# Kernel optimization log

Measured on AMD Instinct MI355X. Metric: run time of the kernel, lower is better.

The kernel has to match this reference:

```python
import jax, jax.numpy as jnp
import numpy as np

ALPHA = 0.1
MAX_ITER = 35
TOL = 0.01
STEP = ALPHA / 2.0  # step_size = alpha/2 as in TV2DFunction.forward


def _prox_tv1d(step, y):
    """Exact 1D TV prox via taut-string lower/upper hulls (faithful port of _prox_tv1d)."""
    n = y.shape[0]
    width = n + 1
    dt = y.dtype
    cs = jnp.cumsum(y)
    y_low = jnp.concatenate([jnp.zeros(1, dt), cs - step]).at[width - 1].add(step)
    y_up = jnp.concatenate([jnp.zeros(1, dt), cs + step]).at[width - 1].add(-step)

    inf = jnp.asarray(jnp.inf, dt)
    il = jnp.zeros(width, jnp.int32)   # index_low
    iu = jnp.zeros(width, jnp.int32)   # index_up
    idx = jnp.zeros(width, jnp.int32)  # breakpoint indices
    sl = jnp.zeros(width, dt).at[0].set(inf)    # slope_low
    su = jnp.zeros(width, dt).at[0].set(-inf)   # slope_up
    z = jnp.zeros(width, dt)
    zero = jnp.int32(0)

    def fdiv(num, a, b):
        # a > b always holds on the taken branch; maximum() only guards the
        # unselected jnp.where branch against NaN/Inf.
        return num / jnp.maximum(a - b, 1).astype(dt)

    def body(i, st):
        il, sl, iu, su, idx, z, s_l, c_l, s_u, c_u, c = st
        c_l = c_l + 1
        c_u = c_u + 1
        il = il.at[c_l].set(i)
        iu = iu.at[c_u].set(i)
        sl = sl.at[c_l].set(y_low[i] - y_low[i - 1])

        def w1_cond(t):
            il_, sl_, c_l_ = t
            return (c_l_ > s_l + 1) & (sl_[jnp.maximum(s_l, c_l_ - 1)] <= sl_[c_l_])

        def w1_body(t):
            il_, sl_, c_l_ = t
            c_l_ = c_l_ - 1
            il_ = il_.at[c_l_].set(i)
            ns = jnp.where(c_l_ > s_l + 1,
                           fdiv(y_low[i] - y_low[il_[c_l_ - 1]], i, il_[c_l_ - 1]),
                           fdiv(y_low[i] - z[c], i, idx[c]))
            return il_, sl_.at[c_l_].set(ns), c_l_

        il, sl, c_l = jax.lax.while_loop(w1_cond, w1_body, (il, sl, c_l))

        su = su.at[c_u].set(y_up[i] - y_up[i - 1])

        def w2_cond(t):
            iu_, su_, c_u_ = t
            return (c_u_ > s_u + 1) & (su_[jnp.maximum(s_u, c_u_ - 1)] >= su_[c_u_])

        def w2_body(t):
            iu_, su_, c_u_ = t
            c_u_ = c_u_ - 1
            iu_ = iu_.at[c_u_].set(i)
            ns = jnp.where(c_u_ > s_u + 1,
                           fdiv(y_up[i] - y_up[iu_[c_u_ - 1]], i, iu_[c_u_ - 1]),
                           fdiv(y_up[i] - z[c], i, idx[c]))
            return iu_, su_.at[c_u_].set(ns), c_u_

        iu, su, c_u = jax.lax.while_loop(w2_cond, w2_body, (iu, su, c_u))

        def w3_cond(t):
            idx_, z_, sl_, il_, s_u_, c_ = t
            return (c_l == s_l + 1) & (c_u > s_u_ + 1) & (sl_[c_l] >= su[s_u_ + 1])

        def w3_body(t):
            idx_, z_, sl_, il_, s_u_, c_ = t
            c_ = c_ + 1
            s_u_ = s_u_ + 1
            k = iu[s_u_]
            idx_ = idx_.at[c_].set(k)
            z_ = z_.at[c_].set(y_up[k])
            il_ = il_.at[s_l].set(k)
            sl_ = sl_.at[c_l].set(fdiv(y_low[i] - y_up[k], i, k))
            return idx_, z_, sl_, il_, s_u_, c_

        idx, z, sl, il, s_u, c = jax.lax.while_loop(w3_cond, w3_body, (idx, z, sl, il, s_u, c))

        def w4_cond(t):
            idx_, z_, su_, iu_, s_l_, c_ = t
            return (c_u == s_u + 1) & (c_l > s_l_ + 1) & (su_[c_u] <= sl[s_l_ + 1])

        def w4_body(t):
            idx_, z_, su_, iu_, s_l_, c_ = t
            c_ = c_ + 1
            s_l_ = s_l_ + 1
            k = il[s_l_]
            idx_ = idx_.at[c_].set(k)
            z_ = z_.at[c_].set(y_low[k])
            iu_ = iu_.at[s_u].set(k)
            su_ = su_.at[c_u].set(fdiv(y_up[i] - y_low[k], i, k))
            return idx_, z_, su_, iu_, s_l_, c_

        idx, z, su, iu, s_l, c = jax.lax.while_loop(w4_cond, w4_body, (idx, z, su, iu, s_l, c))

        return il, sl, iu, su, idx, z, s_l, c_l, s_u, c_u, c

    st = (il, sl, iu, su, idx, z, zero, zero, zero, zero, zero)
    il, sl, iu, su, idx, z, s_l, c_l, s_u, c_u, c = jax.lax.fori_loop(1, width, body, st)

    # tail: append remaining lower-hull points to the breakpoint list
    m = c_l - s_l
    offs = jnp.arange(width)
    valid = (offs >= 1) & (offs <= m)
    src = il[jnp.clip(s_l + offs, 0, width - 1)]
    tgt = jnp.where(valid, c + offs, width)  # 'width' is out of bounds -> dropped
    idx = idx.at[tgt].set(src, mode='drop')
    z = z.at[tgt].set(y_low[src], mode='drop')
    c = c + m

    # piecewise-constant output: slope of taut string on each segment
    a = (z - jnp.roll(z, 1)) / jnp.maximum(idx - jnp.roll(idx, 1), 1).astype(dt)
    knots = jnp.where(offs <= c, idx, n + 1)  # sorted; idx[c] == n
    seg = jnp.searchsorted(knots, jnp.arange(n), side='right')  # segment id in [1, c]
    return a[seg]


def _prox_cols(step, A):
    return jax.vmap(lambda col: _prox_tv1d(step, col), in_axes=1, out_axes=1)(A)


def _prox_rows(step, A):
    return jax.vmap(lambda row: _prox_tv1d(step, row))(A)


def _prox_tv2d(x, step, max_iter, tol):
    """Douglas-Rachford splitting for 2D TV prox (Barbero & Sra 2014)."""
    def cond(carry):
        it, x_, p, q, acc = carry
        return (it < max_iter) & (acc >= tol)

    def body(carry):
        it, x_, p, q, _ = carry
        y = _prox_cols(step, x_ + p)
        p = p + x_ - y
        x2 = _prox_rows(step, y + q)
        q = q + y - x2
        acc = jnp.max(jnp.abs(y - x2))
        return it + 1, x2, p, q, acc

    z0 = jnp.zeros_like(x)
    init = (jnp.int32(0), x, z0, z0, jnp.asarray(jnp.inf, x.dtype))
    return jax.lax.while_loop(cond, body, init)[1]


def setup_inputs() -> dict:
    key = jax.random.key(0)
    X = jax.random.normal(key, (256, 256), dtype=jnp.float32)
    return {"X": X}


def reference(X):
    return _prox_tv2d(X, STEP, MAX_ITER, TOL)
```

## Files before the change

kernel.cpp:

```cpp
#include <hip/hip_runtime.h>

#define N 256
#define NB 256
#define NT 64
#define LAM 0.05f
#define TWOLAM (2.0f * LAM)
#define FOURLAM (4.0f * LAM)
#define MAXIT 35
#define TOL 0.01f
#define SLOTSTRIDE 2
#define POLLBUDGET (1 << 17)

typedef unsigned long long u64;

__device__ __forceinline__ float rlane(float v, int lane) {
    return __int_as_float(__builtin_amdgcn_readlane(__float_as_int(v), lane));
}

__device__ __forceinline__ void gstore(float* p, float v) {
    __hip_atomic_store(p, v, __ATOMIC_RELAXED, __HIP_MEMORY_SCOPE_AGENT);
}
__device__ __forceinline__ u64 ald(const u64* p) {
    return __hip_atomic_load(p, __ATOMIC_RELAXED, __HIP_MEMORY_SCOPE_AGENT);
}
__device__ __forceinline__ void ast(u64* p, u64 v) {
    __hip_atomic_store(p, v, __ATOMIC_RELAXED, __HIP_MEMORY_SCOPE_AGENT);
}

__device__ __forceinline__ void gload_col(const float* mat, int c, int lane, float& a,
                                          float& b, float& d, float& e) {
    const float* p0 = mat + (size_t)lane * N + c;
    const float* p1 = p0 + 64 * N;
    const float* p2 = p0 + 128 * N;
    const float* p3 = p0 + 192 * N;
    asm volatile("global_load_dword %0, %4, off sc0 sc1\n\t"
                 "global_load_dword %1, %5, off sc0 sc1\n\t"
                 "global_load_dword %2, %6, off sc0 sc1\n\t"
                 "global_load_dword %3, %7, off sc0 sc1\n\t"
                 "s_waitcnt vmcnt(0)"
                 : "=&v"(a), "=&v"(b), "=&v"(d), "=&v"(e)
                 : "v"(p0), "v"(p1), "v"(p2), "v"(p3)
                 : "memory");
}

struct Dist { float r0, r1, r2, r3; };

__device__ __forceinline__ float dfetch(const Dist& d, int k) {
    const int lane = k & 63;
    const int sel = k >> 6;
    float a = rlane(d.r0, lane);
    float b = rlane(d.r1, lane);
    float c = rlane(d.r2, lane);
    float e = rlane(d.r3, lane);
    float ab = (sel & 1) ? b : a;
    float ce = (sel & 1) ? e : c;
    return (sel & 2) ? ce : ab;
}

__device__ __forceinline__ void flushseg(Dist& o, int lo, int hi, float val, int lane) {
    const unsigned len = (unsigned)(hi - lo);
    const int base = lane - lo;
    o.r0 = ((unsigned)(base      ) <= len) ? val : o.r0;
    o.r1 = ((unsigned)(base + 64 ) <= len) ? val : o.r1;
    o.r2 = ((unsigned)(base + 128) <= len) ? val : o.r2;
    o.r3 = ((unsigned)(base + 192) <= len) ? val : o.r3;
}

__device__ __forceinline__ u64 sel4(u64 a, u64 b, u64 c, u64 d, int r) {
    u64 ab = (r & 1) ? b : a;
    u64 cd = (r & 1) ? d : c;
    return (r & 2) ? cd : ab;
}

__device__ __forceinline__ unsigned wredmax(unsigned x) {
    unsigned t;
    t = (unsigned)__builtin_amdgcn_update_dpp(0, (int)x, 0x111, 0xf, 0xf, true); x = x > t ? x : t;
    t = (unsigned)__builtin_amdgcn_update_dpp(0, (int)x, 0x112, 0xf, 0xf, true); x = x > t ? x : t;
    t = (unsigned)__builtin_amdgcn_update_dpp(0, (int)x, 0x114, 0xf, 0xf, true); x = x > t ? x : t;
    t = (unsigned)__builtin_amdgcn_update_dpp(0, (int)x, 0x118, 0xf, 0xf, true); x = x > t ? x : t;
    t = (unsigned)__builtin_amdgcn_update_dpp(0, (int)x, 0x142, 0xf, 0xf, true); x = x > t ? x : t;
    t = (unsigned)__builtin_amdgcn_update_dpp(0, (int)x, 0x143, 0xf, 0xf, true); x = x > t ? x : t;
    return (unsigned)__builtin_amdgcn_readlane((int)x, 63);
}

__device__ __forceinline__ void pollcol(const u64* m, int c, unsigned seq, int lane, Dist& v) {
    const u64* p0 = m + (size_t)lane * N + c;
    const u64* p1 = p0 + 64 * N;
    const u64* p2 = p0 + 128 * N;
    const u64* p3 = p0 + 192 * N;
    u64 f0 = ald(p0), f1 = ald(p1), f2 = ald(p2), f3 = ald(p3);
    int spin = 0;
    for (;;) {
        u64 g0 = ald(p0), g1 = ald(p1), g2 = ald(p2), g3 = ald(p3);
        const bool ok = ((unsigned)f0 >= seq) & ((unsigned)f1 >= seq) &
                        ((unsigned)f2 >= seq) & ((unsigned)f3 >= seq);
        if (__all((int)ok)) break;
        if (__builtin_expect(++spin > POLLBUDGET, 0)) break;
        f0 = g0; f1 = g1; f2 = g2; f3 = g3;
    }
    v.r0 = __uint_as_float((unsigned)(f0 >> 32));
    v.r1 = __uint_as_float((unsigned)(f1 >> 32));
    v.r2 = __uint_as_float((unsigned)(f2 >> 32));
    v.r3 = __uint_as_float((unsigned)(f3 >> 32));
}

__device__ __forceinline__ void storerow(u64* m, int row, unsigned seq, const Dist& o, int lane) {
    u64* r = m + (size_t)row * N;
    ast(r + lane,       ((u64)__float_as_uint(o.r0) << 32) | (u64)seq);
    ast(r + lane + 64,  ((u64)__float_as_uint(o.r1) << 32) | (u64)seq);
    ast(r + lane + 128, ((u64)__float_as_uint(o.r2) << 32) | (u64)seq);
    ast(r + lane + 192, ((u64)__float_as_uint(o.r3) << 32) | (u64)seq);
}

__device__ void tv1d_scan(const Dist& v, Dist& o, const int lane)
{
    const float lam = LAM, mlam = -LAM, twolam = TWOLAM;

    Dist vnx;
    {
        float a0 = __shfl_down(v.r0, 1), a1 = __shfl_down(v.r1, 1);
        float a2 = __shfl_down(v.r2, 1), a3 = __shfl_down(v.r3, 1);
        const bool hi = (lane == 63);
        vnx.r0 = hi ? rlane(v.r1, 0) : a0;
        vnx.r1 = hi ? rlane(v.r2, 0) : a1;
        vnx.r2 = hi ? rlane(v.r3, 0) : a2;
        vnx.r3 = hi ? v.r3 : a3;
    }
    Dist d;
    d.r0 = vnx.r0 - v.r0;  d.r1 = vnx.r1 - v.r1;
    d.r2 = vnx.r2 - v.r2;  d.r3 = vnx.r3 - v.r3;
    const unsigned lambits = __float_as_uint(lam);
    Dist sl;
    sl.r0 = __uint_as_float((__float_as_uint(d.r0) & 0x80000000u) | lambits);
    sl.r1 = __uint_as_float((__float_as_uint(d.r1) & 0x80000000u) | lambits);
    sl.r2 = __uint_as_float((__float_as_uint(d.r2) & 0x80000000u) | lambits);
    sl.r3 = __uint_as_float((__float_as_uint(d.r3) & 0x80000000u) | lambits);
    Dist slp;
    {
        float b0 = __shfl_up(sl.r0, 1), b1 = __shfl_up(sl.r1, 1);
        float b2 = __shfl_up(sl.r2, 1), b3 = __shfl_up(sl.r3, 1);
        const bool lo = (lane == 0);
        slp.r0 = lo ? 0.0f : b0;
        slp.r1 = lo ? rlane(sl.r0, 63) : b1;
        slp.r2 = lo ? rlane(sl.r1, 63) : b2;
        slp.r3 = lo ? rlane(sl.r2, 63) : b3;
    }
    Dist e, g;
    {
        float t0 = v.r0 - slp.r0, t1 = v.r1 - slp.r1, t2 = v.r2 - slp.r2, t3 = v.r3 - slp.r3;
        e.r0 = t0 + sl.r0;  e.r1 = t1 + sl.r1;  e.r2 = t2 + sl.r2;  e.r3 = t3 + sl.r3;
        g.r0 = t0 - lam;    g.r1 = t1 - lam;    g.r2 = t2 - lam;    g.r3 = t3 - lam;
    }
    const u64 S0 = __ballot(d.r0 < 0.0f);
    const u64 S1 = __ballot(d.r1 < 0.0f);
    const u64 S2 = __ballot(d.r2 < 0.0f);
    const u64 S3 = __ballot(d.r3 < 0.0f);
    const u64 B20 = __ballot(fabsf(d.r0) > TWOLAM);
    const u64 B21 = __ballot(fabsf(d.r1) > TWOLAM);
    const u64 B22 = __ballot(fabsf(d.r2) > TWOLAM);
    const u64 B23 = __ballot(fabsf(d.r3) > TWOLAM);
    const u64 B40 = __ballot(fabsf(d.r0) > FOURLAM);
    const u64 B41 = __ballot(fabsf(d.r1) > FOURLAM);
    const u64 B42 = __ballot(fabsf(d.r2) > FOURLAM);
    const u64 B43 = __ballot(fabsf(d.r3) > FOURLAM);
    const u64 Sp0 = (S0 << 1);
    const u64 Sp1 = (S1 << 1) | (S0 >> 63);
    const u64 Sp2 = (S2 << 1) | (S1 >> 63);
    const u64 Sp3 = (S3 << 1) | (S2 >> 63);
    const u64 NF0 = ~(B40 | (B20 & ~(S0 ^ Sp0)));
    const u64 NF1 = ~(B41 | (B21 & ~(S1 ^ Sp1)));
    const u64 NF2 = ~(B42 | (B22 & ~(S2 ^ Sp2)));
    const u64 NF3 = ~((B43 | (B23 & ~(S3 ^ Sp3))) & 0x7FFFFFFFFFFFFFFFull);
    const u64 FNn0 = (S0 & B20) | (~S0 & B40);
    const u64 FNn1 = (S1 & B21) | (~S1 & B41);
    const u64 FNn2 = (S2 & B22) | (~S2 & B42);
    const u64 FNn3 = (S3 & B23) | (~S3 & B43);
    const u64 FNp0 = (~S0 & B20) | (S0 & B40);
    const u64 FNp1 = (~S1 & B21) | (S1 & B41);
    const u64 FNp2 = (~S2 & B22) | (S2 & B42);
    const u64 FNp3 = (~S3 & B23) | (S3 & B43);
    const int initFF = (int)(B40 & 1ull);

    auto firstnf = [&](int jmin) -> int {
        const int w = jmin >> 6;
        u64 m = sel4(NF0, NF1, NF2, NF3, w) >> (jmin & 63);
        if (m) return jmin + (int)__builtin_ctzll(m);
        u64 m1 = (w < 1) ? NF1 : 0ull;
        u64 m2 = (w < 2) ? NF2 : 0ull;
        if (m1) return 64 + (int)__builtin_ctzll(m1);
        if (m2) return 128 + (int)__builtin_ctzll(m2);
        return 192 + (int)__builtin_ctzll(NF3);
    };

    auto trigbit = [&](int kk, int neg) -> int {
        const int w = kk >> 6;
        const u64 m = neg ? sel4(FNn0, FNn1, FNn2, FNn3, w)
                          : sel4(FNp0, FNp1, FNp2, FNp3, w);
        return (int)((m >> (kk & 63)) & 1ull);
    };

    int k = 0, k0 = 0, km = 0, kp = 0;
    float umin = lam, umax = mlam;
    const float v0 = rlane(v.r0, 0);
    float vmin = v0 - lam, vmax = v0 + lam;
    float flen = 1.0f;
    float rnext = 0.5f;
    float vn1 = rlane(vnx.r0, 0);

    auto fastfwd = [&]() {
        const int K1 = firstnf(k + 1);
        const int sneg = (int)((sel4(S0, S1, S2, S3, k >> 6) >> (k & 63)) & 1ull);
        flushseg(o, k, k, sneg ? vmin : vmax, lane);
        if (K1 > k + 1) {
            const int lo = k + 1;
            const unsigned len = (unsigned)(K1 - 1 - lo);
            const int base = lane - lo;
            o.r0 = ((unsigned)(base      ) <= len) ? e.r0 : o.r0;
            o.r1 = ((unsigned)(base + 64 ) <= len) ? e.r1 : o.r1;
            o.r2 = ((unsigned)(base + 128) <= len) ? e.r2 : o.r2;
            o.r3 = ((unsigned)(base + 192) <= len) ? e.r3 : o.r3;
        }
        k = K1; k0 = K1; km = K1; kp = K1;
        vmin = dfetch(g, K1);
        vmax = vmin + twolam;
        umin = lam; umax = mlam;
        flen = 1.0f; rnext = 0.5f;
        vn1 = dfetch(vnx, K1);
    };

    auto do_step = [&]() {
        const float un = umin + vn1 - vmin;
        const float ux = umax + vn1 - vmax;
        const bool neg = un < mlam;
        const bool pos = ux > lam;
        const int wn = (k + 1) >> 6, bn = (k + 1) & 63;
        const int tn = (int)((sel4(FNn0, FNn1, FNn2, FNn3, wn) >> bn) & 1ull);
        const int tp = (int)((sel4(FNp0, FNp1, FNp2, FNp3, wn) >> bn) & 1ull);
        if (__builtin_expect((int)(neg | pos), 1)) {
            const float fval = neg ? vmin : vmax;
            const int   fhi  = neg ? km : kp;
            flushseg(o, k0, fhi, fval, lane);
            const int k0n = fhi + 1;
            float vstar;
            int trig;
            if (__builtin_expect((int)(k0n <= k), 0)) {
                vstar = dfetch(v, k0n);
                trig = trigbit(k0n, (int)neg);
            } else {
                vstar = vn1;
                trig = neg ? tn : tp;
            }
            k = k0n; k0 = k0n; km = k0n; kp = k0n;
            vmin = neg ? vstar : vstar - twolam;
            vmax = vmin + twolam;
            umin = lam; umax = mlam;
            flen = 1.0f; rnext = 0.5f;
            if (k < N - 1 && trig) {
                fastfwd();
            } else {
                vn1 = dfetch(vnx, k);
            }
        } else {
            k++;
            const float r = rnext;
            flen += 1.0f;
            const bool cmin = (un >= lam);
            const bool cmax = (ux <= mlam);
            vmin = cmin ? fmaf(un - lam, r, vmin) : vmin;
            km   = cmin ? k : km;
            umin = cmin ? lam : un;
            vmax = cmax ? fmaf(ux + lam, r, vmax) : vmax;
            kp   = cmax ? k : kp;
            umax = cmax ? mlam : ux;
            vn1 = dfetch(vnx, k);
            rnext = __builtin_amdgcn_rcpf(flen + 1.0f);
        }
    };

    if (initFF) fastfwd();

    for (;;) {
        while (k < N - 1) {
            do_step();
            if (k >= N - 1) break;
            do_step();
        }
        for (;;) {
            if (umin < 0.0f) {
                flushseg(o, k0, km, vmin, lane);
                k0 = km + 1;
                if (k0 > N - 1) return;
                km = k = k0;
                vmin = dfetch(v, k0);
                umin = lam;
                umax = vmin + lam - vmax;
                flen = 1.0f;
            } else if (umax > 0.0f) {
                flushseg(o, k0, kp, vmax, lane);
                k0 = kp + 1;
                if (k0 > N - 1) return;
                kp = k = k0;
                vmax = dfetch(v, k0);
                umax = mlam;
                umin = vmax - lam - vmin;
                flen = 1.0f;
            } else {
                vmin += umin / flen;
                flushseg(o, k0, k, vmin, lane);
                return;
            }
            if (k != N - 1) break;
        }
        rnext = 0.5f;
        vn1 = dfetch(vnx, k);
    }
}

template <bool WANT>
__device__ __forceinline__ unsigned wavebar(u64* slots, unsigned seq,
                                            unsigned payload, int line, int lane)
{
    __builtin_amdgcn_s_waitcnt(0);
    __hip_atomic_store(&slots[line * SLOTSTRIDE],
                       ((u64)payload << 32) | (u64)seq,
                       __ATOMIC_RELAXED, __HIP_MEMORY_SCOPE_AGENT);
    auto ld = [&](int i) {
        return __hip_atomic_load(&slots[i * SLOTSTRIDE],
                                 __ATOMIC_RELAXED, __HIP_MEMORY_SCOPE_AGENT);
    };
    u64 f0 = ld(lane), f1 = ld(lane + 64), f2 = ld(lane + 128), f3 = ld(lane + 192);
    int spin = 0;
    for (;;) {
        u64 g0 = ld(lane), g1 = ld(lane + 64), g2 = ld(lane + 128), g3 = ld(lane + 192);
        const bool ok = ((unsigned)f0 >= seq) & ((unsigned)f1 >= seq) &
                        ((unsigned)f2 >= seq) & ((unsigned)f3 >= seq);
        if (__all((int)ok)) break;
        if (__builtin_expect(++spin > POLLBUDGET, 0)) break;
        f0 = g0; f1 = g1; f2 = g2; f3 = g3;
    }
    unsigned ga = 0u;
    if (WANT) {
        unsigned a = (unsigned)(f0 >> 32), b = (unsigned)(f1 >> 32);
        unsigned c = (unsigned)(f2 >> 32), d = (unsigned)(f3 >> 32);
        a = a > b ? a : b;  c = c > d ? c : d;  a = a > c ? a : c;
        ga = wredmax(a);
    }
    return ga;
}

__global__ __launch_bounds__(NT) void tv2d_half(const float* __restrict__ X,
                                                float* __restrict__ xw,
                                                u64* __restrict__ ytg,
                                                u64* __restrict__ slots)
{
    const int lane = threadIdx.x;
    const int b = blockIdx.x;

    Dist p = {0.f, 0.f, 0.f, 0.f};
    Dist q = {0.f, 0.f, 0.f, 0.f};

    for (int it = 0; it < MAXIT; ++it) {
        const float* xs = (it == 0) ? X : xw;
        Dist v, o;
        gload_col(xs, b, lane, v.r0, v.r1, v.r2, v.r3);
        v.r0 += p.r0;  v.r1 += p.r1;  v.r2 += p.r2;  v.r3 += p.r3;
        tv1d_scan(v, o, lane);
        p.r0 = v.r0 - o.r0;  p.r1 = v.r1 - o.r1;
        p.r2 = v.r2 - o.r2;  p.r3 = v.r3 - o.r3;
        storerow(ytg, b, (unsigned)(it + 1), o, lane);

        Dist yv, w, o2;
        pollcol(ytg, b, (unsigned)(it + 1), lane, yv);
        w.r0 = yv.r0 + q.r0;
        w.r1 = yv.r1 + q.r1;
        w.r2 = yv.r2 + q.r2;
        w.r3 = yv.r3 + q.r3;
        tv1d_scan(w, o2, lane);
        q.r0 = w.r0 - o2.r0;  q.r1 = w.r1 - o2.r1;
        q.r2 = w.r2 - o2.r2;  q.r3 = w.r3 - o2.r3;
        float* xr = xw + (size_t)b * N;
        gstore(xr + lane,       o2.r0);
        gstore(xr + lane + 64,  o2.r1);
        gstore(xr + lane + 128, o2.r2);
        gstore(xr + lane + 192, o2.r3);

        float am = fmaxf(fmaxf(fabsf(yv.r0 - o2.r0), fabsf(yv.r1 - o2.r1)),
                         fmaxf(fabsf(yv.r2 - o2.r2), fabsf(yv.r3 - o2.r3)));
        const unsigned amu = wredmax(__float_as_uint(am));

        if (it == MAXIT - 1) break;

        const unsigned ga = wavebar<true>(slots, (unsigned)(it + 1), amu, b, lane);
        if (__uint_as_float(ga) < TOL) break;
    }
}

__global__ __launch_bounds__(NT) void tv2d_coop(const float* __restrict__ X,
                                                float* __restrict__ xw,
                                                float* __restrict__ yt,
                                                u64* __restrict__ slots)
{
    const int lane = threadIdx.x;
    const int b = blockIdx.x;

    Dist p = {0.f, 0.f, 0.f, 0.f};
    Dist q = {0.f, 0.f, 0.f, 0.f};
    unsigned accprev = 0u;

    for (int it = 0; it < MAXIT; ++it) {
        const float* xs = (it == 0) ? X : xw;
        Dist v, o;
        gload_col(xs, b, lane, v.r0, v.r1, v.r2, v.r3);
        v.r0 += p.r0;  v.r1 += p.r1;  v.r2 += p.r2;  v.r3 += p.r3;
        tv1d_scan(v, o, lane);
        p.r0 = v.r0 - o.r0;  p.r1 = v.r1 - o.r1;
        p.r2 = v.r2 - o.r2;  p.r3 = v.r3 - o.r3;
        float* yr = yt + b * N;
        gstore(yr + lane,       o.r0);
        gstore(yr + lane + 64,  o.r1);
        gstore(yr + lane + 128, o.r2);
        gstore(yr + lane + 192, o.r3);
        wavebar<false>(slots, 2u * (unsigned)it + 1u, accprev, b, lane);

        Dist yv, w, o2;
        gload_col(yt, b, lane, yv.r0, yv.r1, yv.r2, yv.r3);
        w.r0 = yv.r0 + q.r0;
        w.r1 = yv.r1 + q.r1;
        w.r2 = yv.r2 + q.r2;
        w.r3 = yv.r3 + q.r3;
        tv1d_scan(w, o2, lane);
        float d0 = yv.r0 - o2.r0;
        float d1 = yv.r1 - o2.r1;
        float d2 = yv.r2 - o2.r2;
        float d3 = yv.r3 - o2.r3;
        q.r0 = w.r0 - o2.r0;  q.r1 = w.r1 - o2.r1;
        q.r2 = w.r2 - o2.r2;  q.r3 = w.r3 - o2.r3;
        float* xr = xw + b * N;
        gstore(xr + lane,       o2.r0);
        gstore(xr + lane + 64,  o2.r1);
        gstore(xr + lane + 128, o2.r2);
        gstore(xr + lane + 192, o2.r3);

        float am = fmaxf(fmaxf(fabsf(d0), fabsf(d1)), fmaxf(fabsf(d2), fabsf(d3)));
        const unsigned amu = wredmax(__float_as_uint(am));

        if (it == MAXIT - 1) break;

        const unsigned ga = wavebar<true>(slots, 2u * (unsigned)it + 2u, amu, b, lane);
        if (__uint_as_float(ga) < TOL) break;
        accprev = amu;
    }
}

extern "C" void kernel_launch(void* const* d_in, const int* in_sizes, int n_in,
                              void* d_out, int out_size, void* d_ws, size_t ws_size,
                              hipStream_t stream) {
    const float* X = (const float*)d_in[0];
    float* xw = (float*)d_out;

    const size_t need = (size_t)N * N * sizeof(u64)
                      + (size_t)N * SLOTSTRIDE * sizeof(u64);
    if (ws_size >= need) {
        u64* ytg   = (u64*)d_ws;
        u64* slots = ytg + (size_t)N * N;
        (void)hipMemsetAsync(d_ws, 0, need, stream);
        void* args[] = { (void*)&X, (void*)&xw, (void*)&ytg, (void*)&slots };
        (void)hipLaunchCooperativeKernel((void*)tv2d_half, dim3(NB), dim3(NT), args, 0, stream);
    } else {
        float* yt = (float*)d_ws;
        u64* slots = (u64*)((char*)d_ws + (size_t)N * N * sizeof(float));
        (void)hipMemsetAsync((void*)slots, 0, N * SLOTSTRIDE * sizeof(u64), stream);
        void* args[] = { (void*)&X, (void*)&xw, (void*)&yt, (void*)&slots };
        (void)hipLaunchCooperativeKernel((void*)tv2d_coop, dim3(NB), dim3(NT), args, 0, stream);
    }
}
```

Measured before the change: 272.0 us.

## Replace x-phase global barrier with sequence-tagged per-element polling for row data

Adds a kernel that publishes the row-prox output x as sequence-tagged 64-bit words, the same way y is already tagged. The next iteration's column pass can then poll for exactly the data it needs instead of reading a plain buffer after a full barrier. The per-iteration barrier now only carries the convergence reduction and skips the waitcnt drain, and the output is written once at the end. This costs twice the workspace and wider 64-bit traffic. Correctness now depends on every column read seeing its tag, and the poll budget is also lowered.

After: 274.0 us. No clear change (+0.8%).

```diff
diff --git a/kernel.cpp b/kernel.cpp
--- a/kernel.cpp
+++ b/kernel.cpp
@@ -9,7 +9,7 @@
 #define MAXIT 35
 #define TOL 0.01f
 #define SLOTSTRIDE 2
-#define POLLBUDGET (1 << 17)
+#define POLLBUDGET (1 << 15)
 
 typedef unsigned long long u64;
 
@@ -316,11 +316,11 @@
     }
 }
 
-template <bool WANT>
+template <bool WANT, bool DRAIN>
 __device__ __forceinline__ unsigned wavebar(u64* slots, unsigned seq,
                                             unsigned payload, int line, int lane)
 {
-    __builtin_amdgcn_s_waitcnt(0);
+    if (DRAIN) __builtin_amdgcn_s_waitcnt(0);
     __hip_atomic_store(&slots[line * SLOTSTRIDE],
                        ((u64)payload << 32) | (u64)seq,
                        __ATOMIC_RELAXED, __HIP_MEMORY_SCOPE_AGENT);
@@ -348,6 +348,62 @@
     return ga;
 }
 
+__global__ __launch_bounds__(NT) void tv2d_tag(const float* __restrict__ X,
+                                               float* __restrict__ out,
+                                               u64* __restrict__ ytg,
+                                               u64* __restrict__ xwg,
+                                               u64* __restrict__ slots)
+{
+    const int lane = threadIdx.x;
+    const int b = blockIdx.x;
+
+    Dist p = {0.f, 0.f, 0.f, 0.f};
+    Dist q = {0.f, 0.f, 0.f, 0.f};
+    Dist xout = {0.f, 0.f, 0.f, 0.f};
+
+    for (int it = 0; it < MAXIT; ++it) {
+        Dist v, o;
+        if (it == 0) {
+            gload_col(X, b, lane, v.r0, v.r1, v.r2, v.r3);
+        } else {
+            pollcol(xwg, b, (unsigned)it, lane, v);
+        }
+        v.r0 += p.r0;  v.r1 += p.r1;  v.r2 += p.r2;  v.r3 += p.r3;
+        tv1d_scan(v, o, lane);
+        p.r0 = v.r0 - o.r0;  p.r1 = v.r1 - o.r1;
+        p.r2 = v.r2 - o.r2;  p.r3 = v.r3 - o.r3;
+        storerow(ytg, b, (unsigned)(it + 1), o, lane);
+
+        Dist yv, w, o2;
+        pollcol(ytg, b, (unsigned)(it + 1), lane, yv);
+        w.r0 = yv.r0 + q.r0;
+        w.r1 = yv.r1 + q.r1;
+        w.r2 = yv.r2 + q.r2;
+        w.r3 = yv.r3 + q.r3;
+        tv1d_scan(w, o2, lane);
+        q.r0 = w.r0 - o2.r0;  q.r1 = w.r1 - o2.r1;
+        q.r2 = w.r2 - o2.r2;  q.r3 = w.r3 - o2.r3;
+        xout = o2;
+
+        float am = fmaxf(fmaxf(fabsf(yv.r0 - o2.r0), fabsf(yv.r1 - o2.r1)),
+                         fmaxf(fabsf(yv.r2 - o2.r2), fabsf(yv.r3 - o2.r3)));
+        const unsigned amu = wredmax(__float_as_uint(am));
+
+        if (it == MAXIT - 1) break;
+
+        storerow(xwg, b, (unsigned)(it + 1), o2, lane);
+
+        const unsigned ga = wavebar<true, false>(slots, (unsigned)(it + 1), amu, b, lane);
+        if (__uint_as_float(ga) < TOL) break;
+    }
+
+    float* xr = out + (size_t)b * N;
+    xr[lane]       = xout.r0;
+    xr[lane + 64]  = xout.r1;
+    xr[lane + 128] = xout.r2;
+    xr[lane + 192] = xout.r3;
+}
+
 __global__ __launch_bounds__(NT) void tv2d_half(const float* __restrict__ X,
                                                 float* __restrict__ xw,
                                                 u64* __restrict__ ytg,
@@ -390,65 +446,8 @@
 
         if (it == MAXIT - 1) break;
 
-        const unsigned ga = wavebar<true>(slots, (unsigned)(it + 1), amu, b, lane);
+        const unsigned ga = wavebar<true, true>(slots, (unsigned)(it + 1), amu, b, lane);
         if (__uint_as_float(ga) < TOL) break;
-    }
-}
-
-__global__ __launch_bounds__(NT) void tv2d_coop(const float* __restrict__ X,
-                                                float* __restrict__ xw,
-                                                float* __restrict__ yt,
-                                                u64* __restrict__ slots)
-{
-    const int lane = threadIdx.x;
-    const int b = blockIdx.x;
-
-    Dist p = {0.f, 0.f, 0.f, 0.f};
-    Dist q = {0.f, 0.f, 0.f, 0.f};
-    unsigned accprev = 0u;
-
-    for (int it = 0; it < MAXIT; ++it) {
-        const float* xs = (it == 0) ? X : xw;
-        Dist v, o;
-        gload_col(xs, b, lane, v.r0, v.r1, v.r2, v.r3);
-        v.r0 += p.r0;  v.r1 += p.r1;  v.r2 += p.r2;  v.r3 += p.r3;
-        tv1d_scan(v, o, lane);
-        p.r0 = v.r0 - o.r0;  p.r1 = v.r1 - o.r1;
-        p.r2 = v.r2 - o.r2;  p.r3 = v.r3 - o.r3;
-        float* yr = yt + b * N;
-        gstore(yr + lane,       o.r0);
-        gstore(yr + lane + 64,  o.r1);
-        gstore(yr + lane + 128, o.r2);
-        gstore(yr + lane + 192, o.r3);
-        wavebar<false>(slots, 2u * (unsigned)it + 1u, accprev, b, lane);
-
-        Dist yv, w, o2;
-        gload_col(yt, b, lane, yv.r0, yv.r1, yv.r2, yv.r3);
-        w.r0 = yv.r0 + q.r0;
-        w.r1 = yv.r1 + q.r1;
-        w.r2 = yv.r2 + q.r2;
-        w.r3 = yv.r3 + q.r3;
-        tv1d_scan(w, o2, lane);
-        float d0 = yv.r0 - o2.r0;
-        float d1 = yv.r1 - o2.r1;
-        float d2 = yv.r2 - o2.r2;
-        float d3 = yv.r3 - o2.r3;
-        q.r0 = w.r0 - o2.r0;  q.r1 = w.r1 - o2.r1;
-        q.r2 = w.r2 - o2.r2;  q.r3 = w.r3 - o2.r3;
-        float* xr = xw + b * N;
-        gstore(xr + lane,       o2.r0);
-        gstore(xr + lane + 64,  o2.r1);
-        gstore(xr + lane + 128, o2.r2);
-        gstore(xr + lane + 192, o2.r3);
-
-        float am = fmaxf(fmaxf(fabsf(d0), fabsf(d1)), fmaxf(fabsf(d2), fabsf(d3)));
-        const unsigned amu = wredmax(__float_as_uint(am));
-
-        if (it == MAXIT - 1) break;
-
-        const unsigned ga = wavebar<true>(slots, 2u * (unsigned)it + 2u, amu, b, lane);
-        if (__uint_as_float(ga) < TOL) break;
-        accprev = amu;
     }
 }
 
@@ -458,19 +457,21 @@
     const float* X = (const float*)d_in[0];
     float* xw = (float*)d_out;
 
-    const size_t need = (size_t)N * N * sizeof(u64)
+    const size_t need = (size_t)2 * N * N * sizeof(u64)
                       + (size_t)N * SLOTSTRIDE * sizeof(u64);
     if (ws_size >= need) {
         u64* ytg   = (u64*)d_ws;
+        u64* xwg   = ytg + (size_t)N * N;
+        u64* slots = xwg + (size_t)N * N;
+        (void)hipMemsetAsync(d_ws, 0, need, stream);
+        void* args[] = { (void*)&X, (void*)&xw, (void*)&ytg, (void*)&xwg, (void*)&slots };
+        (void)hipLaunchCooperativeKernel((void*)tv2d_tag, dim3(NB), dim3(NT), args, 0, stream);
+    } else {
+        u64* ytg   = (u64*)d_ws;
         u64* slots = ytg + (size_t)N * N;
-        (void)hipMemsetAsync(d_ws, 0, need, stream);
+        (void)hipMemsetAsync(d_ws, 0, (size_t)N * N * sizeof(u64)
+                                     + (size_t)N * SLOTSTRIDE * sizeof(u64), stream);
         void* args[] = { (void*)&X, (void*)&xw, (void*)&ytg, (void*)&slots };
         (void)hipLaunchCooperativeKernel((void*)tv2d_half, dim3(NB), dim3(NT), args, 0, stream);
-    } else {
-        float* yt = (float*)d_ws;
-        u64* slots = (u64*)((char*)d_ws + (size_t)N * N * sizeof(float));
-        (void)hipMemsetAsync((void*)slots, 0, N * SLOTSTRIDE * sizeof(u64), stream);
-        void* args[] = { (void*)&X, (void*)&xw, (void*)&yt, (void*)&slots };
-        (void)hipLaunchCooperativeKernel((void*)tv2d_coop, dim3(NB), dim3(NT), args, 0, stream);
-    }
-}
+    }
+}
```
